# Optimization experiments

Hardware: AMD Instinct MI355X
Metric: run time of the kernel (lower is better)

## Reference

```python
import jax, jax.numpy as jnp
import numpy as np

HEADS = 12
WINDOW = 128
EPS = 1e-5
MAX_WAVELENGTH = 10000.0
MASK_VALUE = -10000.0


def rms_norm(x, gamma):
    # keras LayerNormalization(rms_scaling=True): x * rsqrt(mean(x^2)+eps) * gamma
    return x * jax.lax.rsqrt(jnp.mean(jnp.square(x), axis=-1, keepdims=True) + EPS) * gamma


def rope(x):
    # x: [B, S, H, D]; keras_hub RotaryEmbedding (rotate-half, freqs tiled twice)
    S, D = x.shape[1], x.shape[-1]
    inv_freq = 1.0 / (MAX_WAVELENGTH ** (jnp.arange(0, D, 2, dtype=jnp.float32) / D))
    freqs = jnp.arange(S, dtype=jnp.float32)[:, None] * inv_freq[None, :]  # [S, D/2]
    emb = jnp.concatenate([freqs, freqs], axis=-1)  # [S, D]
    cos = jnp.cos(emb)[None, :, None, :]
    sin = jnp.sin(emb)[None, :, None, :]
    half = jnp.concatenate([-x[..., D // 2:], x[..., : D // 2]], axis=-1)
    return x * cos + half * sin


def setup_inputs() -> dict:
    key = jax.random.key(0)
    ks = jax.random.split(key, 8)
    B, S, Dm, Di = 2, 4096, 768, 1152
    return {
        "x": jax.random.normal(ks[0], (B, S, Dm), dtype=jnp.float32),
        "padding_mask": jnp.ones((B, S), dtype=jnp.int32),
        "w_qkv": jax.random.normal(ks[1], (Dm, 3 * Dm), dtype=jnp.float32) * 0.02,
        "w_o": jax.random.normal(ks[2], (Dm, Dm), dtype=jnp.float32) * 0.02,
        "gamma_attn": jnp.ones((Dm,), dtype=jnp.float32),
        "gamma_mlp": jnp.ones((Dm,), dtype=jnp.float32),
        "w_i0": jax.random.normal(ks[3], (Dm, Di), dtype=jnp.float32) * 0.02,
        "w_i1": jax.random.normal(ks[4], (Dm, Di), dtype=jnp.float32) * 0.02,
        "w_mo": jax.random.normal(ks[5], (Di, Dm), dtype=jnp.float32) * 0.02,
    }


def reference(x, padding_mask, w_qkv, w_o, gamma_attn, gamma_mlp, w_i0, w_i1, w_mo):
    B, S, Dm = x.shape
    H = HEADS
    Dh = Dm // H

    # --- attention block ---
    res = x
    h = rms_norm(x, gamma_attn)
    qkv = (h @ w_qkv).reshape(B, S, 3, H, Dh)
    q, k, v = qkv[:, :, 0], qkv[:, :, 1], qkv[:, :, 2]  # [B,S,H,Dh]
    q = rope(q)
    k = rope(k)
    scale = jnp.sqrt(jnp.asarray(Dh, dtype=x.dtype))
    scores = jnp.einsum("bqhd,bkhd->bhqk", q, k) / scale  # [B,H,S,S]

    idx = jnp.arange(S)
    sw_mask = (jnp.abs(idx[:, None] - idx[None, :]) <= WINDOW // 2).astype(x.dtype)
    scores = scores + (1.0 - sw_mask)[None, None, :, :] * MASK_VALUE
    p_mask = padding_mask.astype(x.dtype)[:, None, None, :]
    scores = scores + (1.0 - p_mask) * MASK_VALUE

    attn = jax.nn.softmax(scores.astype(jnp.float32), axis=-1).astype(x.dtype)
    out = jnp.einsum("bhqk,bkhd->bqhd", attn, v).reshape(B, S, Dm)
    x = res + out @ w_o

    # --- GeGLU MLP block ---
    res = x
    h = rms_norm(x, gamma_mlp)
    gate = jax.nn.gelu(h @ w_i0, approximate=True)
    x = res + (gate * (h @ w_i1)) @ w_mo
    return x
```

## Files before the change

### kernel.cpp

```cpp
#include <hip/hip_runtime.h>
#include <hip/hip_bf16.h>
#include <math.h>

#define SEQ   4096
#define BATCH 2
#define DM    768
#define DI    1152
#define NHEAD 12
#define DH    64
#define NTOK  (BATCH * SEQ)
#define HALFW 64

typedef unsigned short u16;
typedef __attribute__((ext_vector_type(8))) short   short8;
typedef __attribute__((ext_vector_type(4))) float   f32x4;
typedef __attribute__((ext_vector_type(8))) unsigned short ushort8;

__device__ __forceinline__ u16 f2bf(float f) {
    unsigned int u = __float_as_uint(f);
    u += 0x7fffu + ((u >> 16) & 1u);
    return (u16)(u >> 16);
}
__device__ __forceinline__ float bf2f(u16 b) {
    return __uint_as_float(((unsigned int)b) << 16);
}

__device__ __forceinline__ void gload16(const void* g, void* l) {
    __builtin_amdgcn_global_load_lds(
        (const __attribute__((address_space(1))) void*)g,
        (__attribute__((address_space(3))) void*)l, 16, 0, 0);
}

__device__ __forceinline__ float gelu_tanh(float v) {
    return 0.5f * v * (1.0f + tanhf(0.7978845608028654f * (v + 0.044715f * v * v * v)));
}

__global__ __launch_bounds__(256)
void wtrans_kernel(const float* __restrict__ W, u16* __restrict__ WT, int K, int N) {
    __shared__ float S[32][33];
    const int tn = blockIdx.x, tk = blockIdx.y;
    const int tx = threadIdx.x & 31, ty = threadIdx.x >> 5;
    #pragma unroll
    for (int i = 0; i < 4; ++i) {
        const int r = ty + i * 8;
        S[r][tx] = W[(size_t)(tk * 32 + r) * N + tn * 32 + tx];
    }
    __syncthreads();
    #pragma unroll
    for (int i = 0; i < 4; ++i) {
        const int r = ty + i * 8;
        WT[(size_t)(tn * 32 + r) * K + tk * 32 + tx] = f2bf(S[tx][r]);
    }
}

__global__ __launch_bounds__(256)
void rope_table_kernel(float* __restrict__ cosT, float* __restrict__ sinT) {
    const int id = blockIdx.x * 256 + threadIdx.x;
    const int j = id & 31, s = id >> 5;
    const float inv = powf(10000.0f, -(float)j * (1.0f / 32.0f));
    const float ph = (float)s * inv;
    cosT[id] = cosf(ph);
    sinT[id] = sinf(ph);
}

__global__ __launch_bounds__(256)
void rmsnorm_kernel(const float* __restrict__ x, const float* __restrict__ g,
                    u16* __restrict__ out) {
    const int row = blockIdx.x;
    const int t = threadIdx.x;
    const float* xr = x + (size_t)row * DM;
    float a = xr[t], b = xr[t + 256], c = xr[t + 512];
    float ss = a * a + b * b + c * c;
    #pragma unroll
    for (int o = 32; o > 0; o >>= 1) ss += __shfl_xor(ss, o);
    __shared__ float red[4];
    if ((t & 63) == 0) red[t >> 6] = ss;
    __syncthreads();
    float tot = red[0] + red[1] + red[2] + red[3];
    float inv = 1.0f / sqrtf(tot * (1.0f / DM) + 1e-5f);
    u16* orow = out + (size_t)row * DM;
    orow[t]       = f2bf(a * inv * g[t]);
    orow[t + 256] = f2bf(b * inv * g[t + 256]);
    orow[t + 512] = f2bf(c * inv * g[t + 512]);
}

template<int EPI, bool RES, bool OBF, bool DUAL>
__global__ __launch_bounds__(256)
void bgemm_kernel(const u16* __restrict__ A, const u16* __restrict__ B,
                  const u16* __restrict__ B2, void* __restrict__ Cv,
                  const float* __restrict__ R, int M, int N, int K) {
    __shared__ u16 As[4096];
    __shared__ u16 Bs[4096];
    __shared__ u16 B2s[DUAL ? 4096 : 2];
    const int t = threadIdx.x;
    const int w = t >> 6, l = t & 63;
    const int wm = w >> 1, wn = w & 1;
    const int bm = blockIdx.y, bn = blockIdx.x;

    const int s0 = (w * 2 + 0) * 64 + l;
    const int s1 = (w * 2 + 1) * 64 + l;
    const int am0 = s0 >> 2, ak0 = ((s0 & 3) ^ ((s0 >> 3) & 3)) * 8;
    const int am1 = s1 >> 2, ak1 = ((s1 & 3) ^ ((s1 >> 3) & 3)) * 8;
    const u16* aSrc0 = A + (size_t)(bm * 128 + am0) * K + ak0;
    const u16* aSrc1 = A + (size_t)(bm * 128 + am1) * K + ak1;
    const u16* bSrc0 = B + (size_t)(bn * 128 + am0) * K + ak0;
    const u16* bSrc1 = B + (size_t)(bn * 128 + am1) * K + ak1;
    const u16* cSrc0 = DUAL ? B2 + (size_t)(bn * 128 + am0) * K + ak0 : nullptr;
    const u16* cSrc1 = DUAL ? B2 + (size_t)(bn * 128 + am1) * K + ak1 : nullptr;
    u16* aDst0 = As + (size_t)(w * 2 + 0) * 512;
    u16* aDst1 = As + (size_t)(w * 2 + 1) * 512;
    u16* bDst0 = Bs + (size_t)(w * 2 + 0) * 512;
    u16* bDst1 = Bs + (size_t)(w * 2 + 1) * 512;
    u16* cDst0 = DUAL ? B2s + (size_t)(w * 2 + 0) * 512 : nullptr;
    u16* cDst1 = DUAL ? B2s + (size_t)(w * 2 + 1) * 512 : nullptr;

    const int lm = l & 15, lk = l >> 4;
    const int xoff = ((lk ^ ((lm >> 1) & 3)) * 16);
    const char* Abase = (const char*)As;
    const char* Bbase = (const char*)Bs;
    const char* Cbase = (const char*)B2s;

    f32x4 acc[4][4] = {};
    f32x4 acc2[4][4] = {};

    const int nk = K >> 5;
    for (int kt = 0; kt < nk; ++kt) {
        gload16(aSrc0, aDst0);
        gload16(aSrc1, aDst1);
        gload16(bSrc0, bDst0);
        gload16(bSrc1, bDst1);
        if (DUAL) { gload16(cSrc0, cDst0); gload16(cSrc1, cDst1); }
        aSrc0 += 32; aSrc1 += 32; bSrc0 += 32; bSrc1 += 32;
        if (DUAL) { cSrc0 += 32; cSrc1 += 32; }
        __syncthreads();

        short8 af[4], bfr[4], cfr[4];
        #pragma unroll
        for (int i = 0; i < 4; ++i) {
            af[i]  = *(const short8*)(Abase + (wm * 64 + i * 16 + lm) * 64 + xoff);
            bfr[i] = *(const short8*)(Bbase + (wn * 64 + i * 16 + lm) * 64 + xoff);
            if (DUAL) cfr[i] = *(const short8*)(Cbase + (wn * 64 + i * 16 + lm) * 64 + xoff);
        }
        #pragma unroll
        for (int i = 0; i < 4; ++i)
            #pragma unroll
            for (int j = 0; j < 4; ++j) {
                acc[i][j] = __builtin_amdgcn_mfma_f32_16x16x32_bf16(af[i], bfr[j], acc[i][j], 0, 0, 0);
                if (DUAL)
                    acc2[i][j] = __builtin_amdgcn_mfma_f32_16x16x32_bf16(af[i], cfr[j], acc2[i][j], 0, 0, 0);
            }
        __syncthreads();
    }

    const int lg = l >> 4;
    float* Cf = (float*)Cv;
    u16*   Cb = (u16*)Cv;
    #pragma unroll
    for (int i = 0; i < 4; ++i) {
        const size_t row0 = (size_t)bm * 128 + wm * 64 + i * 16 + lg * 4;
        #pragma unroll
        for (int j = 0; j < 4; ++j) {
            const size_t col = (size_t)bn * 128 + wn * 64 + j * 16 + lm;
            #pragma unroll
            for (int r = 0; r < 4; ++r) {
                const size_t idx = (row0 + r) * (size_t)N + col;
                float v = acc[i][j][r];
                if (EPI == 3) v = gelu_tanh(v) * acc2[i][j][r];
                if (RES)      v += R[idx];
                if (OBF) Cb[idx] = f2bf(v);
                else     Cf[idx] = v;
            }
        }
    }
}

__device__ __forceinline__ u16* ldsAddr(u16* base, int row, int col) {
    const int ch = (col >> 3) ^ (row & 7);
    return base + row * 64 + ch * 8 + (col & 7);
}

__global__ __launch_bounds__(256)
void attn_kernel(const u16* __restrict__ qkv, const int* __restrict__ pmask,
                 const float* __restrict__ cosT, const float* __restrict__ sinT,
                 u16* __restrict__ out) {
    const int qt = blockIdx.x, h = blockIdx.y, b = blockIdx.z;
    const int q0 = qt * 64;
    const int t = threadIdx.x;
    const int w = t >> 6, l = t & 63;
    const int lm = l & 15, lg = l >> 4;

    __shared__ u16 Qs[64 * 64];
    __shared__ u16 Ks[64 * 64];
    __shared__ u16 Vt[64 * 64];
    __shared__ u16 Ps[64 * 64];

    {
        const int r = t >> 2, j0 = (t & 3) * 8;
        const int s = q0 + r;
        const u16* qrow = qkv + (size_t)(b * SEQ + s) * (3 * DM) + h * DH;
        ushort8 lo = *(const ushort8*)(qrow + j0);
        ushort8 hi = *(const ushort8*)(qrow + j0 + 32);
        const float* cr = cosT + (size_t)s * 32 + j0;
        const float* sr = sinT + (size_t)s * 32 + j0;
        ushort8 olo, ohi;
        #pragma unroll
        for (int e = 0; e < 8; ++e) {
            float c = cr[e], sn = sr[e];
            float xl = bf2f(lo[e]), xh = bf2f(hi[e]);
            olo[e] = f2bf(xl * c - xh * sn);
            ohi[e] = f2bf(xh * c + xl * sn);
        }
        *(ushort8*)ldsAddr(Qs, r, j0)      = olo;
        *(ushort8*)ldsAddr(Qs, r, j0 + 32) = ohi;
    }

    f32x4 oacc[4] = {};
    float Mrun[4], Lrun[4];
    #pragma unroll
    for (int r = 0; r < 4; ++r) { Mrun[r] = -3.0e38f; Lrun[r] = 0.f; }

    for (int kb = 0; kb < 3; ++kb) {
        const int kstart = q0 - 64 + kb * 64;
        __syncthreads();
        {
            const int r = t >> 2, j0 = (t & 3) * 8;
            const int kg = kstart + r;
            ushort8 olo = {}, ohi = {};
            if (kg >= 0 && kg < SEQ) {
                const u16* krow = qkv + (size_t)(b * SEQ + kg) * (3 * DM) + DM + h * DH;
                ushort8 lo = *(const ushort8*)(krow + j0);
                ushort8 hi = *(const ushort8*)(krow + j0 + 32);
                const float* cr = cosT + (size_t)kg * 32 + j0;
                const float* sr = sinT + (size_t)kg * 32 + j0;
                #pragma unroll
                for (int e = 0; e < 8; ++e) {
                    float c = cr[e], sn = sr[e];
                    float xl = bf2f(lo[e]), xh = bf2f(hi[e]);
                    olo[e] = f2bf(xl * c - xh * sn);
                    ohi[e] = f2bf(xh * c + xl * sn);
                }
            }
            *(ushort8*)ldsAddr(Ks, r, j0)      = olo;
            *(ushort8*)ldsAddr(Ks, r, j0 + 32) = ohi;
        }
        {
            const int key = l;
            const int kg = kstart + key;
            const int d0 = w * 16;
            if (kg >= 0 && kg < SEQ) {
                const u16* vrow = qkv + (size_t)(b * SEQ + kg) * (3 * DM) + 2 * DM + h * DH + d0;
                ushort8 v0 = *(const ushort8*)(vrow);
                ushort8 v1 = *(const ushort8*)(vrow + 8);
                #pragma unroll
                for (int e = 0; e < 8; ++e) {
                    *ldsAddr(Vt, d0 + e, key)     = v0[e];
                    *ldsAddr(Vt, d0 + 8 + e, key) = v1[e];
                }
            } else {
                #pragma unroll
                for (int e = 0; e < 16; ++e) *ldsAddr(Vt, d0 + e, key) = 0;
            }
        }
        __syncthreads();

        short8 af[2];
        #pragma unroll
        for (int ks = 0; ks < 2; ++ks)
            af[ks] = *(const short8*)ldsAddr(Qs, w * 16 + lm, ks * 32 + lg * 8);
        f32x4 sacc[4];
        #pragma unroll
        for (int j = 0; j < 4; ++j) {
            f32x4 z = {};
            #pragma unroll
            for (int ks = 0; ks < 2; ++ks) {
                short8 kf = *(const short8*)ldsAddr(Ks, j * 16 + lm, ks * 32 + lg * 8);
                z = __builtin_amdgcn_mfma_f32_16x16x32_bf16(af[ks], kf, z, 0, 0, 0);
            }
            sacc[j] = z;
        }

        float p[4][4];
        int pmj[4], kgj[4];
        #pragma unroll
        for (int j = 0; j < 4; ++j) {
            kgj[j] = kstart + j * 16 + lm;
            pmj[j] = (kgj[j] >= 0 && kgj[j] < SEQ) ? pmask[b * SEQ + kgj[j]] : 0;
        }
        float mt[4] = {-3.0e38f, -3.0e38f, -3.0e38f, -3.0e38f};
        #pragma unroll
        for (int j = 0; j < 4; ++j)
            #pragma unroll
            for (int r = 0; r < 4; ++r) {
                const int qg = q0 + w * 16 + lg * 4 + r;
                const int diff = qg - kgj[j];
                float v = sacc[j][r] * 0.125f;
                const bool valid = (pmj[j] != 0) && (diff <= HALFW) && (diff >= -HALFW);
                v = valid ? v : -3.0e38f;
                p[j][r] = v;
                mt[r] = fmaxf(mt[r], v);
            }

        #pragma unroll
        for (int r = 0; r < 4; ++r) {
            float m = mt[r];
            m = fmaxf(m, __shfl_xor(m, 1));
            m = fmaxf(m, __shfl_xor(m, 2));
            m = fmaxf(m, __shfl_xor(m, 4));
            m = fmaxf(m, __shfl_xor(m, 8));
            const float Mnew = fmaxf(Mrun[r], m);
            float ps = 0.f;
            #pragma unroll
            for (int j = 0; j < 4; ++j) {
                float e = (p[j][r] > -1.0e37f) ? expf(p[j][r] - Mnew) : 0.0f;
                p[j][r] = e; ps += e;
            }
            ps += __shfl_xor(ps, 1); ps += __shfl_xor(ps, 2);
            ps += __shfl_xor(ps, 4); ps += __shfl_xor(ps, 8);
            const float scale = expf(Mrun[r] - Mnew);
            Lrun[r] = Lrun[r] * scale + ps;
            Mrun[r] = Mnew;
            #pragma unroll
            for (int jd = 0; jd < 4; ++jd) oacc[jd][r] *= scale;
        }

        #pragma unroll
        for (int j = 0; j < 4; ++j)
            #pragma unroll
            for (int r = 0; r < 4; ++r)
                *ldsAddr(Ps, w * 16 + lg * 4 + r, j * 16 + lm) = f2bf(p[j][r]);

        #pragma unroll
        for (int ks = 0; ks < 2; ++ks) {
            short8 pa = *(const short8*)ldsAddr(Ps, w * 16 + lm, ks * 32 + lg * 8);
            #pragma unroll
            for (int jd = 0; jd < 4; ++jd) {
                short8 vb = *(const short8*)ldsAddr(Vt, jd * 16 + lm, ks * 32 + lg * 8);
                oacc[jd] = __builtin_amdgcn_mfma_f32_16x16x32_bf16(pa, vb, oacc[jd], 0, 0, 0);
            }
        }
    }

    #pragma unroll
    for (int r = 0; r < 4; ++r) {
        const float inv = (Lrun[r] > 0.f) ? 1.0f / Lrun[r] : 0.0f;
        const size_t row = (size_t)(b * SEQ + q0 + w * 16 + lg * 4 + r);
        #pragma unroll
        for (int jd = 0; jd < 4; ++jd)
            out[row * DM + h * DH + jd * 16 + lm] = f2bf(oacc[jd][r] * inv);
    }
}

extern "C" void kernel_launch(void* const* d_in, const int* in_sizes, int n_in,
                              void* d_out, int out_size, void* d_ws, size_t ws_size,
                              hipStream_t stream) {
    const float* x      = (const float*)d_in[0];
    const int*   pmask  = (const int*)  d_in[1];
    const float* w_qkv  = (const float*)d_in[2];
    const float* w_o    = (const float*)d_in[3];
    const float* g_attn = (const float*)d_in[4];
    const float* g_mlp  = (const float*)d_in[5];
    const float* w_i0   = (const float*)d_in[6];
    const float* w_i1   = (const float*)d_in[7];
    const float* w_mo   = (const float*)d_in[8];
    float* out = (float*)d_out;

    char* ws = (char*)d_ws;
    u16* Wqkv = (u16*)ws;                ws += (size_t)768 * 2304 * 2;
    u16* Wo   = (u16*)ws;                ws += (size_t)768 * 768 * 2;
    u16* Wi0  = (u16*)ws;                ws += (size_t)768 * 1152 * 2;
    u16* Wi1  = (u16*)ws;                ws += (size_t)768 * 1152 * 2;
    u16* Wmo  = (u16*)ws;                ws += (size_t)1152 * 768 * 2;
    u16* hB    = (u16*)ws;               ws += (size_t)NTOK * DM * 2;
    u16* qkvB  = (u16*)ws;               ws += (size_t)NTOK * 3 * DM * 2;
    u16* attnB = (u16*)ws;               ws += (size_t)NTOK * DM * 2;
    u16* prodB = (u16*)ws;               ws += (size_t)NTOK * DI * 2;
    float* ropeCos = (float*)ws;         ws += (size_t)SEQ * 32 * 4;
    float* ropeSin = (float*)ws;         ws += (size_t)SEQ * 32 * 4;

    rope_table_kernel<<<SEQ * 32 / 256, 256, 0, stream>>>(ropeCos, ropeSin);
    wtrans_kernel<<<dim3(2304 / 32, 768 / 32), 256, 0, stream>>>(w_qkv, Wqkv, 768, 2304);
    wtrans_kernel<<<dim3(768 / 32, 768 / 32),  256, 0, stream>>>(w_o,   Wo,   768, 768);
    wtrans_kernel<<<dim3(1152 / 32, 768 / 32), 256, 0, stream>>>(w_i0,  Wi0,  768, 1152);
    wtrans_kernel<<<dim3(1152 / 32, 768 / 32), 256, 0, stream>>>(w_i1,  Wi1,  768, 1152);
    wtrans_kernel<<<dim3(768 / 32, 1152 / 32), 256, 0, stream>>>(w_mo,  Wmo,  1152, 768);

    rmsnorm_kernel<<<NTOK, 256, 0, stream>>>(x, g_attn, hB);
    bgemm_kernel<0, false, true, false><<<dim3(2304 / 128, NTOK / 128), 256, 0, stream>>>(
        hB, Wqkv, nullptr, qkvB, nullptr, NTOK, 2304, 768);
    attn_kernel<<<dim3(SEQ / 64, NHEAD, BATCH), 256, 0, stream>>>(
        qkvB, pmask, ropeCos, ropeSin, attnB);
    bgemm_kernel<0, true, false, false><<<dim3(768 / 128, NTOK / 128), 256, 0, stream>>>(
        attnB, Wo, nullptr, out, x, NTOK, 768, 768);
    rmsnorm_kernel<<<NTOK, 256, 0, stream>>>(out, g_mlp, hB);
    bgemm_kernel<3, false, true, true><<<dim3(1152 / 128, NTOK / 128), 256, 0, stream>>>(
        hB, Wi0, Wi1, prodB, nullptr, NTOK, 1152, 768);
    bgemm_kernel<0, true, false, false><<<dim3(768 / 128, NTOK / 128), 256, 0, stream>>>(
        prodB, Wmo, nullptr, out, out, NTOK, 768, 1152);
}
```

Measured before the change: 372.0 us.

## Double-buffer GEMM LDS tiles and remap blocks across XCDs

The bf16 GEMM kernel now keeps two LDS stages for A, B and B2 and issues the next k-tile's global-to-LDS loads before the current tile's MFMAs, removing one barrier per iteration so loads can overlap compute. Launches switch to a 1D grid, and the block index is remapped so consecutive tile IDs land on the same XCD (assuming round-robin dispatch over 8 XCDs), aiming for better L2 reuse of shared A/B tiles. The cost is twice the LDS, up to 48KB in the dual GEMM, which may reduce occupancy.

```diff
diff --git a/kernel.cpp b/kernel.cpp
--- a/kernel.cpp
+++ b/kernel.cpp
@@ -88,14 +88,20 @@
 __global__ __launch_bounds__(256)
 void bgemm_kernel(const u16* __restrict__ A, const u16* __restrict__ B,
                   const u16* __restrict__ B2, void* __restrict__ Cv,
-                  const float* __restrict__ R, int M, int N, int K) {
-    __shared__ u16 As[4096];
-    __shared__ u16 Bs[4096];
-    __shared__ u16 B2s[DUAL ? 4096 : 2];
+                  const float* __restrict__ R, int M, int N, int K, int nbn) {
+    __shared__ u16 As[2 * 4096];
+    __shared__ u16 Bs[2 * 4096];
+    __shared__ u16 B2s[DUAL ? 2 * 4096 : 2];
     const int t = threadIdx.x;
     const int w = t >> 6, l = t & 63;
     const int wm = w >> 1, wn = w & 1;
-    const int bm = blockIdx.y, bn = blockIdx.x;
+
+    const int nb = gridDim.x;
+    const int orig = blockIdx.x;
+    const int qq = nb >> 3, rr = nb & 7;
+    const int xcd = orig & 7, cidx = orig >> 3;
+    const int wgid = (xcd < rr ? xcd * (qq + 1) : rr * (qq + 1) + (xcd - rr) * qq) + cidx;
+    const int bm = wgid / nbn, bn = wgid % nbn;
 
     const int s0 = (w * 2 + 0) * 64 + l;
     const int s1 = (w * 2 + 1) * 64 + l;
@@ -107,33 +113,36 @@
     const u16* bSrc1 = B + (size_t)(bn * 128 + am1) * K + ak1;
     const u16* cSrc0 = DUAL ? B2 + (size_t)(bn * 128 + am0) * K + ak0 : nullptr;
     const u16* cSrc1 = DUAL ? B2 + (size_t)(bn * 128 + am1) * K + ak1 : nullptr;
-    u16* aDst0 = As + (size_t)(w * 2 + 0) * 512;
-    u16* aDst1 = As + (size_t)(w * 2 + 1) * 512;
-    u16* bDst0 = Bs + (size_t)(w * 2 + 0) * 512;
-    u16* bDst1 = Bs + (size_t)(w * 2 + 1) * 512;
-    u16* cDst0 = DUAL ? B2s + (size_t)(w * 2 + 0) * 512 : nullptr;
-    u16* cDst1 = DUAL ? B2s + (size_t)(w * 2 + 1) * 512 : nullptr;
+    const int dS0 = (w * 2 + 0) * 512;
+    const int dS1 = (w * 2 + 1) * 512;
 
     const int lm = l & 15, lk = l >> 4;
     const int xoff = ((lk ^ ((lm >> 1) & 3)) * 16);
-    const char* Abase = (const char*)As;
-    const char* Bbase = (const char*)Bs;
-    const char* Cbase = (const char*)B2s;
 
     f32x4 acc[4][4] = {};
     f32x4 acc2[4][4] = {};
 
     const int nk = K >> 5;
+
+#define STAGE(pp)  do {                                                        \
+        u16* a_ = As + (pp) * 4096;  u16* b_ = Bs + (pp) * 4096;               \
+        gload16(aSrc0, a_ + dS0);  gload16(aSrc1, a_ + dS1);                   \
+        gload16(bSrc0, b_ + dS0);  gload16(bSrc1, b_ + dS1);                   \
+        if (DUAL) { u16* c_ = B2s + (pp) * 4096;                               \
+                    gload16(cSrc0, c_ + dS0);  gload16(cSrc1, c_ + dS1); }     \
+        aSrc0 += 32; aSrc1 += 32; bSrc0 += 32; bSrc1 += 32;                    \
+        if (DUAL) { cSrc0 += 32; cSrc1 += 32; }                                \
+    } while (0)
+
+    STAGE(0);
+    __syncthreads();
+    int p = 0;
     for (int kt = 0; kt < nk; ++kt) {
-        gload16(aSrc0, aDst0);
-        gload16(aSrc1, aDst1);
-        gload16(bSrc0, bDst0);
-        gload16(bSrc1, bDst1);
-        if (DUAL) { gload16(cSrc0, cDst0); gload16(cSrc1, cDst1); }
-        aSrc0 += 32; aSrc1 += 32; bSrc0 += 32; bSrc1 += 32;
-        if (DUAL) { cSrc0 += 32; cSrc1 += 32; }
-        __syncthreads();
-
+        if (kt + 1 < nk) STAGE(p ^ 1);
+
+        const char* Abase = (const char*)As + p * 8192;
+        const char* Bbase = (const char*)Bs + p * 8192;
+        const char* Cbase = (const char*)B2s + p * 8192;
         short8 af[4], bfr[4], cfr[4];
         #pragma unroll
         for (int i = 0; i < 4; ++i) {
@@ -150,7 +159,9 @@
                     acc2[i][j] = __builtin_amdgcn_mfma_f32_16x16x32_bf16(af[i], cfr[j], acc2[i][j], 0, 0, 0);
             }
         __syncthreads();
-    }
+        p ^= 1;
+    }
+#undef STAGE
 
     const int lg = l >> 4;
     float* Cf = (float*)Cv;
@@ -385,15 +396,15 @@
     wtrans_kernel<<<dim3(768 / 32, 1152 / 32), 256, 0, stream>>>(w_mo,  Wmo,  1152, 768);
 
     rmsnorm_kernel<<<NTOK, 256, 0, stream>>>(x, g_attn, hB);
-    bgemm_kernel<0, false, true, false><<<dim3(2304 / 128, NTOK / 128), 256, 0, stream>>>(
-        hB, Wqkv, nullptr, qkvB, nullptr, NTOK, 2304, 768);
+    bgemm_kernel<0, false, true, false><<<(NTOK / 128) * (2304 / 128), 256, 0, stream>>>(
+        hB, Wqkv, nullptr, qkvB, nullptr, NTOK, 2304, 768, 2304 / 128);
     attn_kernel<<<dim3(SEQ / 64, NHEAD, BATCH), 256, 0, stream>>>(
         qkvB, pmask, ropeCos, ropeSin, attnB);
-    bgemm_kernel<0, true, false, false><<<dim3(768 / 128, NTOK / 128), 256, 0, stream>>>(
-        attnB, Wo, nullptr, out, x, NTOK, 768, 768);
+    bgemm_kernel<0, true, false, false><<<(NTOK / 128) * (768 / 128), 256, 0, stream>>>(
+        attnB, Wo, nullptr, out, x, NTOK, 768, 768, 768 / 128);
     rmsnorm_kernel<<<NTOK, 256, 0, stream>>>(out, g_mlp, hB);
-    bgemm_kernel<3, false, true, true><<<dim3(1152 / 128, NTOK / 128), 256, 0, stream>>>(
-        hB, Wi0, Wi1, prodB, nullptr, NTOK, 1152, 768);
-    bgemm_kernel<0, true, false, false><<<dim3(768 / 128, NTOK / 128), 256, 0, stream>>>(
-        prodB, Wmo, nullptr, out, out, NTOK, 768, 1152);
-}
+    bgemm_kernel<3, false, true, true><<<(NTOK / 128) * (1152 / 128), 256, 0, stream>>>(
+        hB, Wi0, Wi1, prodB, nullptr, NTOK, 1152, 768, 1152 / 128);
+    bgemm_kernel<0, true, false, false><<<(NTOK / 128) * (768 / 128), 256, 0, stream>>>(
+        prodB, Wmo, nullptr, out, out, NTOK, 768, 1152, 768 / 128);
+}
```

Result: faster. 332.3 us (-10.7%).
